# Kernel optimization log

Measured on AMD Instinct MI355X. Metric: run time of the kernel, lower is better.

The kernel has to match this reference:

```python
import jax, jax.numpy as jnp
from jax import lax
import numpy as np

# pywt db4 filter bank (ascending order)
DEC_LO = np.array([-0.010597401784997278, 0.032883011666982945, 0.030841381835986965,
                   -0.18703481171888114, -0.02798376941698385, 0.6308807679295904,
                   0.7148465705525415, 0.23037781330885523], dtype=np.float32)
F_LEN = DEC_LO.shape[0]
_signs = ((-1.0) ** (np.arange(F_LEN) + 1)).astype(np.float32)
DEC_HI = _signs * DEC_LO[::-1]
REC_LO = DEC_LO[::-1].copy()
REC_HI = DEC_HI[::-1].copy()
# conv filters flipped -> cross-correlation kernels for lax.conv
DEC_K = np.stack([DEC_LO[::-1], DEC_HI[::-1]])[:, None, :]   # (2, 1, F): lo/hi analysis
REC_K = np.stack([REC_LO[::-1], REC_HI[::-1]])[None, :, :]   # (1, 2, F): synthesis, sums lo+hi
LEVELS = 3


def dwt_level(x, dec_k):
    """One symmetric-mode DWT level. x: (M, n) -> (cA, cD) each (M, floor((n+F-1)/2))."""
    f = dec_k.shape[-1]
    x_ext = jnp.pad(x, ((0, 0), (f - 1, f - 1)), mode='symmetric')[:, 1:]
    y = lax.conv_general_dilated(x_ext[:, None, :], dec_k, (2,), 'VALID',
                                 dimension_numbers=('NCH', 'OIH', 'NCH'))
    return y[:, 0], y[:, 1]


def idwt_level(ca, cd, rec_k, out_len):
    """One IDWT level; trims to out_len (original length at that level)."""
    f = rec_k.shape[-1]
    m, L = ca.shape
    up = jnp.zeros((m, 2, 2 * L), ca.dtype).at[:, 0, ::2].set(ca).at[:, 1, ::2].set(cd)
    y = lax.conv_general_dilated(up, rec_k, (1,), [(f - 1, f - 1)],
                                 dimension_numbers=('NCH', 'OIH', 'NCH'))[:, 0]
    s = f - 2
    return y[:, s:s + out_len]


def setup_inputs() -> dict:
    key = jax.random.key(0)
    B, N, D = 8, 4096, 768
    x = jax.random.normal(key, (B, N, D), dtype=jnp.float32)
    w_approx = jnp.ones((D,), dtype=jnp.float32)
    w_details = jnp.ones((LEVELS, D), dtype=jnp.float32)
    return {"x": x, "w_approx": w_approx, "w_details": w_details}


def reference(x, w_approx, w_details):
    B, N, D = x.shape
    dec_k = jnp.asarray(DEC_K)
    rec_k = jnp.asarray(REC_K)
    # all channels processed at once: (B, N, D) -> (B*D, N)
    sig = x.transpose(0, 2, 1).reshape(B * D, N)
    # J-level decomposition, recording per-level lengths for reconstruction
    a = sig
    lengths = []
    details = []
    for _ in range(LEVELS):
        lengths.append(a.shape[-1])
        a, d = dwt_level(a, dec_k)
        details.append(d)
    # pointwise mixing: one scalar per channel per band (matches ones(1,1,D) param sliced per-channel)
    def chan(w):  # (D,) -> (B*D, 1)
        return jnp.broadcast_to(w, (B, D)).reshape(B * D, 1)
    a = a * chan(w_approx)
    details = [d * chan(w_details[j]) for j, d in enumerate(details)]
    # reconstruction
    rec = a
    for j in reversed(range(LEVELS)):
        rec = idwt_level(rec, details[j], rec_k, lengths[j])
    rec = rec.reshape(B, D, N).transpose(0, 2, 1)
    # residual connection (dropout=0.0)
    return x + rec
```

## Files before the change

kernel.cpp:

```cpp
#include <hip/hip_runtime.h>


namespace {

constexpr int NT  = 256;
constexpr int N0  = 4096;
constexpr int DCH = 768;
constexpr int T   = 256;
constexpr int G   = 8;
constexpr int NDG = DCH / G;
constexpr int L1v = 2051, L2v = 1029, L3v = 518;

constexpr int NINT = 8 * 14 * 3;

constexpr int SP = 972;
constexpr int OX = 0, OA1 = 356, OD1 = 536, OA2 = 716, OD2 = 804,
              OA3 = 892, OD3 = 932, OREC = 716;

__device__ constexpr float LO[8] = {
  -0.010597401784997278f,  0.032883011666982945f,  0.030841381835986965f,
  -0.18703481171888114f,  -0.02798376941698385f,   0.6308807679295904f,
   0.7148465705525415f,    0.23037781330885523f };
__device__ constexpr float HI[8] = {
  -0.23037781330885523f,   0.7148465705525415f,   -0.6308807679295904f,
  -0.02798376941698385f,   0.18703481171888114f,   0.030841381835986965f,
  -0.032883011666982945f, -0.010597401784997278f };
__device__ constexpr float LOF[8] = {
   0.23037781330885523f,   0.7148465705525415f,    0.6308807679295904f,
  -0.02798376941698385f,  -0.18703481171888114f,   0.030841381835986965f,
   0.032883011666982945f, -0.010597401784997278f };
__device__ constexpr float HIF[8] = {
  -0.010597401784997278f, -0.032883011666982945f,  0.030841381835986965f,
   0.18703481171888114f,  -0.02798376941698385f,  -0.6308807679295904f,
   0.7148465705525415f,   -0.23037781330885523f };

__device__ __forceinline__ int refl(int g, int n) {
  g = (g < 0) ? (-g - 1) : g;
  return (g >= n) ? (2 * n - 1 - g) : g;
}

struct Streams {
  float xa[22];
  float a1a[14], d1a[29];
  float a2a[10], d2a[13];
  float a3a[5],  d3a[5];
  float r2a[7],  r1a[11];
};

template <int SMODE>
__device__ __forceinline__ void superstep(Streams& S,
                                          const float* __restrict__ xrow,
                                          float* __restrict__ orow, int bk8,
                                          float wa, float w0, float w1,
                                          float w2) {
#pragma unroll
  for (int i = 0; i < 16; ++i)
    S.xa[6 + i] = xrow[(long)(bk8 - 48 + i) * DCH];

#pragma unroll
  for (int u = 0; u < 2; ++u) {
#pragma unroll
    for (int j = 0; j < 4; ++j) {
      float slo = 0.f, shi = 0.f;
#pragma unroll
      for (int k = 0; k < 8; ++k) {
        const float v = S.xa[8 * u + 2 * j + k];
        slo = fmaf(LOF[k], v, slo);
        shi = fmaf(HIF[k], v, shi);
      }
      S.a1a[6 + 4 * u + j]  = slo;
      S.d1a[21 + 4 * u + j] = w0 * shi;
    }
#pragma unroll
    for (int i = 0; i < 2; ++i) {
      float slo = 0.f, shi = 0.f;
#pragma unroll
      for (int k = 0; k < 8; ++k) {
        const float v = S.a1a[4 * u + 2 * i + k];
        slo = fmaf(LOF[k], v, slo);
        shi = fmaf(HIF[k], v, shi);
      }
      S.a2a[6 + 2 * u + i] = slo;
      S.d2a[9 + 2 * u + i] = w1 * shi;
    }
    {
      float slo = 0.f, shi = 0.f;
#pragma unroll
      for (int k = 0; k < 8; ++k) {
        const float v = S.a2a[2 * u + k];
        slo = fmaf(LOF[k], v, slo);
        shi = fmaf(HIF[k], v, shi);
      }
      S.a3a[3 + u] = wa * slo;
      S.d3a[3 + u] = w2 * shi;
    }
    {
      float e = 0.f, o = 0.f;
#pragma unroll
      for (int m = 0; m < 4; ++m) {
        e = fmaf(LO[2 * m + 1], S.a3a[u + m], e);
        e = fmaf(HI[2 * m + 1], S.d3a[u + m], e);
        o = fmaf(LO[2 * m],     S.a3a[u + m], o);
        o = fmaf(HI[2 * m],     S.d3a[u + m], o);
      }
      S.r2a[3 + 2 * u]     = e;
      S.r2a[3 + 2 * u + 1] = o;
    }
#pragma unroll
    for (int h = 0; h < 2; ++h) {
      float e = 0.f, o = 0.f;
#pragma unroll
      for (int m = 0; m < 4; ++m) {
        e = fmaf(LO[2 * m + 1], S.r2a[2 * u + h + m], e);
        e = fmaf(HI[2 * m + 1], S.d2a[2 * u + h + m], e);
        o = fmaf(LO[2 * m],     S.r2a[2 * u + h + m], o);
        o = fmaf(HI[2 * m],     S.d2a[2 * u + h + m], o);
      }
      S.r1a[3 + 4 * u + 2 * h]     = e;
      S.r1a[3 + 4 * u + 2 * h + 1] = o;
    }
    if (SMODE != 0) {
#pragma unroll
      for (int tau = 0; tau < 4; ++tau) {
        bool doSt;
        if (SMODE == 2)      doSt = true;
        else if (SMODE == 1) doSt = (u == 1) && (tau >= 1);
        else                 doSt = (u == 0) || (tau == 0);
        if (doSt) {
          float e = 0.f, o = 0.f;
#pragma unroll
          for (int m = 0; m < 4; ++m) {
            e = fmaf(LO[2 * m + 1], S.r1a[4 * u + tau + m], e);
            e = fmaf(HI[2 * m + 1], S.d1a[4 * u + tau + m], e);
            o = fmaf(LO[2 * m],     S.r1a[4 * u + tau + m], o);
            o = fmaf(HI[2 * m],     S.d1a[4 * u + tau + m], o);
          }
          const long ofs = bk8 + 8 * u - 90 + 2 * tau;
          orow[ofs * DCH]       = e + xrow[ofs * DCH];
          orow[(ofs + 1) * DCH] = o + xrow[(ofs + 1) * DCH];
        }
      }
    }
  }
#pragma unroll
  for (int i = 0; i < 6; ++i)  S.xa[i]  = S.xa[i + 16];
#pragma unroll
  for (int i = 0; i < 6; ++i)  S.a1a[i] = S.a1a[i + 8];
#pragma unroll
  for (int i = 0; i < 21; ++i) S.d1a[i] = S.d1a[i + 8];
#pragma unroll
  for (int i = 0; i < 6; ++i)  S.a2a[i] = S.a2a[i + 4];
#pragma unroll
  for (int i = 0; i < 9; ++i)  S.d2a[i] = S.d2a[i + 4];
#pragma unroll
  for (int i = 0; i < 3; ++i) { S.a3a[i] = S.a3a[i + 2]; S.d3a[i] = S.d3a[i + 2]; }
#pragma unroll
  for (int i = 0; i < 3; ++i)  S.r2a[i] = S.r2a[i + 4];
#pragma unroll
  for (int i = 0; i < 3; ++i)  S.r1a[i] = S.r1a[i + 8];
}


__device__ void analyze_g(const float* __restrict__ in, int Oin,
                          float* __restrict__ oa, float* __restrict__ od,
                          int cnt, int Oout, int lenout, int i2) {
  for (int p = i2; p < cnt; p += 32) {
    const int gp = refl(Oout + p, lenout);
    const int qb = 2 * gp - 6 - Oin;
    float alo = 0.f, ahi = 0.f;
#pragma unroll
    for (int k = 0; k < 8; ++k) {
      const float v = in[qb + k];
      alo = fmaf(LOF[k], v, alo);
      ahi = fmaf(HIF[k], v, ahi);
    }
    oa[p] = alo;
    od[p] = ahi;
  }
}

__device__ void synth_g(const float* __restrict__ ca,
                        const float* __restrict__ cd, int doff,
                        float* __restrict__ o, float sa, float sd, int npair,
                        int i2) {
  for (int t = i2; t < npair; t += 32) {
    float e = 0.f, ed = 0.f, oe = 0.f, od_ = 0.f;
#pragma unroll
    for (int m = 0; m < 4; ++m) {
      e   = fmaf(LO[2 * m + 1], ca[t + m], e);
      ed  = fmaf(HI[2 * m + 1], cd[t + doff + m], ed);
      oe  = fmaf(LO[2 * m],     ca[t + m], oe);
      od_ = fmaf(HI[2 * m],     cd[t + doff + m], od_);
    }
    o[2 * t]     = sa * e  + sd * ed;
    o[2 * t + 1] = sa * oe + sd * od_;
  }
}

}

__global__ __launch_bounds__(NT) void wavemix_kernel(
    const float* __restrict__ x, const float* __restrict__ wap,
    const float* __restrict__ wdet, float* __restrict__ out) {
  __shared__ float pool[G * SP];
  const int blk = blockIdx.x;
  const int tid = threadIdx.x;

  if (blk < NINT) {
    const int wgroup = blk % 3;
    const int rest   = blk / 3;
    const int s      = 1 + rest % 14;
    const int b      = rest / 14;
    const int n0     = s * T;
    const int d      = wgroup * 256 + tid;

    const float* __restrict__ xrow = x   + ((size_t)b * N0 + n0) * DCH + d;
    float* __restrict__       orow = out + ((size_t)b * N0 + n0) * DCH + d;
    const float wa = wap[d];
    const float w0 = wdet[d];
    const float w1 = wdet[DCH + d];
    const float w2 = wdet[2 * DCH + d];

    Streams S = {};
    int bk8 = 0;
#pragma unroll 1
    for (int m = 0; m < 5; ++m) {
      superstep<0>(S, xrow, orow, bk8, wa, w0, w1, w2);
      bk8 += 16;
    }
    superstep<1>(S, xrow, orow, bk8, wa, w0, w1, w2);
    bk8 += 16;
#pragma unroll 1
    for (int m = 0; m < 15; ++m) {
      superstep<2>(S, xrow, orow, bk8, wa, w0, w1, w2);
      bk8 += 16;
    }
    superstep<3>(S, xrow, orow, bk8, wa, w0, w1, w2);
  } else {
    const int e    = blk - NINT;
    const int nt   = (e & 1) ? 15 : 0;
    const int rest = e >> 1;
    const int dg   = rest % NDG;
    const int b    = rest / NDG;
    const int n0   = nt * T;
    const int d0   = dg * G;

    const size_t base = (size_t)b * N0 * DCH + d0;

    {
      const int q  = tid & 1;
      const int pl = tid >> 1;
      for (int p = pl; p < 352; p += 128) {
        const int g = refl(n0 - 46 + p, N0);
        const float4 v = *reinterpret_cast<const float4*>(
            x + ((size_t)b * N0 + g) * DCH + d0 + 4 * q);
        float* dst = pool + (4 * q) * SP + OX + p;
        dst[0]      = v.x;
        dst[SP]     = v.y;
        dst[2 * SP] = v.z;
        dst[3 * SP] = v.w;
      }
    }

    const int c2 = tid >> 5;
    const int i2 = tid & 31;
    float* P = pool + c2 * SP;
    const float wa = wap[d0 + c2];
    const float w2 = wdet[2 * DCH + d0 + c2];
    const float w1 = wdet[1 * DCH + d0 + c2];
    const float w0 = wdet[0 * DCH + d0 + c2];
    __syncthreads();

    analyze_g(P + OX,  n0 - 46,     P + OA1, P + OD1, 172, n0 / 2 - 20, L1v, i2);
    __syncthreads();
    analyze_g(P + OA1, n0 / 2 - 20, P + OA2, P + OD2,  82, n0 / 4 - 6,  L2v, i2);
    __syncthreads();
    analyze_g(P + OA2, n0 / 4 - 6,  P + OA3, P + OD3,  38, n0 / 8,      L3v, i2);
    __syncthreads();
    synth_g(P + OA3, P + OD3, 0, P + OA2, wa,  w2, 35, i2);
    __syncthreads();
    synth_g(P + OA2, P + OD2, 6, P + OA1, 1.f, w1, 66, i2);
    __syncthreads();
    for (int t = i2; t < 128; t += 32) {
      const float* pa = P + OA1;
      const float* pd = P + OD1;
      float e2 = 0.f, ed = 0.f, oe = 0.f, od_ = 0.f;
#pragma unroll
      for (int m = 0; m < 4; ++m) {
        e2  = fmaf(LO[2 * m + 1], pa[t + m], e2);
        ed  = fmaf(HI[2 * m + 1], pd[t + 20 + m], ed);
        oe  = fmaf(LO[2 * m],     pa[t + m], oe);
        od_ = fmaf(HI[2 * m],     pd[t + 20 + m], od_);
      }
      (P + OREC)[2 * t]     = e2 + w0 * ed  + (P + OX)[2 * t + 46];
      (P + OREC)[2 * t + 1] = oe + w0 * od_ + (P + OX)[2 * t + 47];
    }
    __syncthreads();

    {
      const int c = tid & 7;
      const int j = tid >> 3;
      const float* R = pool + c * SP + OREC;
      float* orow = out + ((size_t)b * N0 + n0) * DCH + d0 + c;
      for (int pos = j; pos < T; pos += 32)
        orow[(size_t)pos * DCH] = R[pos];
    }
  }
}

extern "C" void kernel_launch(void* const* d_in, const int* in_sizes, int n_in,
                              void* d_out, int out_size, void* d_ws, size_t ws_size,
                              hipStream_t stream) {
  const float* x  = (const float*)d_in[0];
  const float* wa = (const float*)d_in[1];
  const float* wd = (const float*)d_in[2];
  float* out      = (float*)d_out;

  const int grid = NINT + 8 * NDG * 2;
  wavemix_kernel<<<grid, NT, 0, stream>>>(x, wa, wd, out);
}
```

Measured before the change: 61.79 us.

## Halve interior segment length, remap block order, batch residual loads

Interior streaming segments shrink from 256 to 128 samples, which doubles the interior block count to spread work over more CUs. The cost is more halo warm-up per output. Block indices are remapped with a stride-8 interleave so that consecutive blocks land on different segments and rows, likely to balance XCD or cache placement. The residual x values for each superstep are loaded up front into a register array instead of being read inline beside each store, so the loads can overlap the computation.

Result: slower. 64.32 us (+4.1%).

```diff
diff --git a/kernel.cpp b/kernel.cpp
--- a/kernel.cpp
+++ b/kernel.cpp
@@ -6,12 +6,14 @@
 constexpr int NT  = 256;
 constexpr int N0  = 4096;
 constexpr int DCH = 768;
-constexpr int T   = 256;
+constexpr int TS  = 128;
+constexpr int TE  = 256;
 constexpr int G   = 8;
 constexpr int NDG = DCH / G;
 constexpr int L1v = 2051, L2v = 1029, L3v = 518;
 
-constexpr int NINT = 8 * 14 * 3;
+constexpr int NSEG = (N0 - 2 * TE) / TS;
+constexpr int NINT = 8 * 3 * NSEG;
 
 constexpr int SP = 972;
 constexpr int OX = 0, OA1 = 356, OD1 = 536, OA2 = 716, OD2 = 804,
@@ -57,6 +59,13 @@
   for (int i = 0; i < 16; ++i)
     S.xa[6 + i] = xrow[(long)(bk8 - 48 + i) * DCH];
 
+  float rres[16];
+  if (SMODE != 0) {
+#pragma unroll
+    for (int i = 0; i < 16; ++i)
+      rres[i] = xrow[(long)(bk8 - 90 + i) * DCH];
+  }
+
 #pragma unroll
   for (int u = 0; u < 2; ++u) {
 #pragma unroll
@@ -136,8 +145,8 @@
             o = fmaf(HI[2 * m],     S.d1a[4 * u + tau + m], o);
           }
           const long ofs = bk8 + 8 * u - 90 + 2 * tau;
-          orow[ofs * DCH]       = e + xrow[ofs * DCH];
-          orow[(ofs + 1) * DCH] = o + xrow[(ofs + 1) * DCH];
+          orow[ofs * DCH]       = e + rres[8 * u + 2 * tau];
+          orow[(ofs + 1) * DCH] = o + rres[8 * u + 2 * tau + 1];
         }
       }
     }
@@ -207,11 +216,12 @@
   const int tid = threadIdx.x;
 
   if (blk < NINT) {
-    const int wgroup = blk % 3;
-    const int rest   = blk / 3;
-    const int s      = 1 + rest % 14;
-    const int b      = rest / 14;
-    const int n0     = s * T;
+    const int wgs    = (blk & 7) * (NINT >> 3) + (blk >> 3);
+    const int si     = wgs % NSEG;
+    const int row    = wgs / NSEG;
+    const int wgroup = row % 3;
+    const int b      = row / 3;
+    const int n0     = (si + 2) * TS;
     const int d      = wgroup * 256 + tid;
 
     const float* __restrict__ xrow = x   + ((size_t)b * N0 + n0) * DCH + d;
@@ -231,7 +241,7 @@
     superstep<1>(S, xrow, orow, bk8, wa, w0, w1, w2);
     bk8 += 16;
 #pragma unroll 1
-    for (int m = 0; m < 15; ++m) {
+    for (int m = 0; m < 7; ++m) {
       superstep<2>(S, xrow, orow, bk8, wa, w0, w1, w2);
       bk8 += 16;
     }
@@ -242,10 +252,8 @@
     const int rest = e >> 1;
     const int dg   = rest % NDG;
     const int b    = rest / NDG;
-    const int n0   = nt * T;
+    const int n0   = nt * TE;
     const int d0   = dg * G;
-
-    const size_t base = (size_t)b * N0 * DCH + d0;
 
     {
       const int q  = tid & 1;
@@ -302,7 +310,7 @@
       const int j = tid >> 3;
       const float* R = pool + c * SP + OREC;
       float* orow = out + ((size_t)b * N0 + n0) * DCH + d0 + c;
-      for (int pos = j; pos < T; pos += 32)
+      for (int pos = j; pos < TE; pos += 32)
         orow[(size_t)pos * DCH] = R[pos];
     }
   }
```
